# Kernel optimization log

Hardware: AMD Instinct MI355X
Metric: run time of the kernel (lower is better)

## Reference

```python
import jax, jax.numpy as jnp
import numpy as np

MARGIN = 0.3
LAMBDA_TRIPLET = 1.0
LAMBDA_ID = 1.0
EPS = 1e-6  # torch pairwise_distance eps added to the difference elementwise


def setup_inputs() -> dict:
    key = jax.random.key(0)
    k1, k2 = jax.random.split(key)
    B, N, D = 64, 512, 512
    reid_features = jax.random.normal(k1, (B, N, D), dtype=jnp.float32)
    # ids in [-1, 32): -1 marks invalid detections, as in the torch module
    track_ids = jax.random.randint(k2, (B, N), -1, 32, dtype=jnp.int32)
    return {"reid_features": reid_features, "track_ids": track_ids}


def _tracking_loss(feats, ids, margin):
    B, N, D = feats.shape
    valid = ids >= 0                                   # (B, N)
    same = ids[:, :, None] == ids[:, None, :]          # (B, N, N)
    not_self = ~jnp.eye(N, dtype=bool)                 # (N, N)
    valid_j = valid[:, None, :]                        # candidates must be valid
    pos_mask = same & not_self & valid_j               # (B, N, N)
    neg_mask = (~same) & valid_j                       # (B, N, N)
    has_pos = pos_mask.any(-1)                         # (B, N)
    has_neg = neg_mask.any(-1)
    enough = valid.sum(-1) >= 2                        # (B,)
    anchor_ok = valid & has_pos & has_neg & enough[:, None]
    # torch.nonzero(mask)[0] == first True index -> argmax on bool
    pos_idx = jnp.argmax(pos_mask, axis=-1)            # (B, N)
    neg_idx = jnp.argmax(neg_mask, axis=-1)
    p = jnp.take_along_axis(feats, pos_idx[..., None], axis=1)  # (B, N, D)
    n = jnp.take_along_axis(feats, neg_idx[..., None], axis=1)
    d_ap = jnp.sqrt(jnp.sum((feats - p + EPS) ** 2, axis=-1))   # (B, N)
    d_an = jnp.sqrt(jnp.sum((feats - n + EPS) ** 2, axis=-1))
    per_anchor = jnp.maximum(d_ap - d_an + margin, 0.0)
    num_triplets = anchor_ok.sum()
    total = jnp.sum(per_anchor * anchor_ok.astype(feats.dtype))
    loss = jnp.where(num_triplets > 0,
                     total / jnp.maximum(num_triplets, 1).astype(feats.dtype),
                     jnp.zeros((), feats.dtype))
    return loss * LAMBDA_TRIPLET


def reference(reid_features, track_ids):
    loss_triplet = _tracking_loss(reid_features, track_ids, MARGIN)
    loss_id = jnp.zeros((), reid_features.dtype)
    tracking_loss = loss_triplet + loss_id
    return tracking_loss, loss_triplet, loss_id
```

## Files before the change

### kernel.cpp

```cpp
#include <hip/hip_runtime.h>

#define MARGIN 0.3f
#define EPS 1e-6f

constexpr int B = 64, N = 512, D = 512;
constexpr int NIDS = 32;

constexpr int MB_THREADS = 256;
constexpr int MB_WAVES = MB_THREADS / 64;
constexpr int ANCH_PER_WAVE = 8;
constexpr int A_BLOCK = MB_WAVES * ANCH_PER_WAVE;
constexpr int MB_BLOCKS = (B * N) / A_BLOCK;


__global__ __launch_bounds__(512) void tl_tables(const int* __restrict__ ids,
                                                 int2* __restrict__ desc,
                                                 int2* __restrict__ hdr) {
    __shared__ int s_ids[N];
    __shared__ int s_first[NIDS], s_second[NIDS];
    __shared__ int s_j0, s_jdiff, s_vcnt;
    const int t = threadIdx.x;
    const int b = blockIdx.x;

    if (t < NIDS) { s_first[t] = N; s_second[t] = N; }
    if (t == 0) { s_j0 = N; s_jdiff = N; s_vcnt = 0; }
    __syncthreads();

    const int v = ids[b * N + t];
    s_ids[t] = v;
    const unsigned long long m = __ballot(v >= 0);
    if ((t & 63) == 0) atomicAdd(&s_vcnt, __popcll(m));
    if (v >= 0) {
        atomicMin(&s_first[v], t);
        atomicMin(&s_j0, t);
    }
    __syncthreads();
    const int id0 = (s_j0 < N) ? s_ids[s_j0] : -2;
    if (v >= 0) {
        if (s_first[v] != t) atomicMin(&s_second[v], t);
        if (v != id0) atomicMin(&s_jdiff, t);
    }
    __syncthreads();

    int2 d = make_int2(-1, -1);
    if (v >= 0 && s_vcnt >= 2) {
        const int posj = (s_first[v] != t) ? s_first[v] : s_second[v];
        const int negj = (v != id0) ? s_j0 : s_jdiff;
        if (posj < N && negj < N) d = make_int2(posj, negj);
    }
    desc[b * N + t] = d;
    if (t == 0) hdr[b] = make_int2(min(s_j0, N - 1), min(s_jdiff, N - 1));
}

__global__ __launch_bounds__(MB_THREADS) void tl_main(const float* __restrict__ feats,
                                                      const int2* __restrict__ desc,
                                                      const int2* __restrict__ hdr,
                                                      float* __restrict__ psum,
                                                      float* __restrict__ pcnt) {
    __shared__ int2 s_desc[A_BLOCK];
    __shared__ float s_wsum[MB_WAVES];
    __shared__ int s_wcnt[MB_WAVES];

    const int t = threadIdx.x;
    const int lane = t & 63;
    const int wave = t >> 6;

    const int logical = ((blockIdx.x & 7) << 7) | (blockIdx.x >> 3);
    const int b = logical >> 4;
    const int seg = (logical & 15) * A_BLOCK;
    const float* __restrict__ bf = feats + (size_t)b * N * D;

    if (t < A_BLOCK) s_desc[t] = desc[b * N + seg + t];

    const int2 h = hdr[b];
    const float4* n0p = (const float4*)(bf + (size_t)h.x * D) + lane * 2;
    const float4* n1p = (const float4*)(bf + (size_t)h.y * D) + lane * 2;
    const float4 n0a = n0p[0], n0b = n0p[1];
    const float4 n1a = n1p[0], n1b = n1p[1];

    __syncthreads();

    float wsum = 0.0f;
    int wcnt = 0;

    #pragma unroll
    for (int c = 0; c < ANCH_PER_WAVE / 4; ++c) {
        const int base = wave * ANCH_PER_WAVE + c * 4;

        int pj[4]; bool okk[4]; bool useN0[4];
        #pragma unroll
        for (int k = 0; k < 4; ++k) {
            const int2 d = s_desc[base + k];
            okk[k] = (d.x >= 0);
            pj[k] = okk[k] ? d.x : 0;
            useN0[k] = (d.y == h.x);
        }

        float4 A0[4], A1[4], P0[4], P1[4];
        #pragma unroll
        for (int k = 0; k < 4; ++k) {
            const int i = seg + base + k;
            const float4* fa = (const float4*)(bf + (size_t)i * D) + lane * 2;
            const float4* fp = (const float4*)(bf + (size_t)pj[k] * D) + lane * 2;
            A0[k] = fa[0]; A1[k] = fa[1];
            P0[k] = fp[0]; P1[k] = fp[1];
        }

        #pragma unroll
        for (int k = 0; k < 4; ++k) {
            const float4 m0 = useN0[k] ? n0a : n1a;
            const float4 m1 = useN0[k] ? n0b : n1b;
            float sap = 0.0f, san = 0.0f, dd;
            dd = A0[k].x - P0[k].x + EPS; sap += dd * dd;
            dd = A0[k].y - P0[k].y + EPS; sap += dd * dd;
            dd = A0[k].z - P0[k].z + EPS; sap += dd * dd;
            dd = A0[k].w - P0[k].w + EPS; sap += dd * dd;
            dd = A1[k].x - P1[k].x + EPS; sap += dd * dd;
            dd = A1[k].y - P1[k].y + EPS; sap += dd * dd;
            dd = A1[k].z - P1[k].z + EPS; sap += dd * dd;
            dd = A1[k].w - P1[k].w + EPS; sap += dd * dd;
            dd = A0[k].x - m0.x + EPS; san += dd * dd;
            dd = A0[k].y - m0.y + EPS; san += dd * dd;
            dd = A0[k].z - m0.z + EPS; san += dd * dd;
            dd = A0[k].w - m0.w + EPS; san += dd * dd;
            dd = A1[k].x - m1.x + EPS; san += dd * dd;
            dd = A1[k].y - m1.y + EPS; san += dd * dd;
            dd = A1[k].z - m1.z + EPS; san += dd * dd;
            dd = A1[k].w - m1.w + EPS; san += dd * dd;

            #pragma unroll
            for (int off = 32; off >= 1; off >>= 1) {
                sap += __shfl_xor(sap, off);
                san += __shfl_xor(san, off);
            }
            const float per = fmaxf(sqrtf(sap) - sqrtf(san) + MARGIN, 0.0f);
            wsum += okk[k] ? per : 0.0f;
            wcnt += okk[k] ? 1 : 0;
        }
    }

    if (lane == 0) { s_wsum[wave] = wsum; s_wcnt[wave] = wcnt; }
    __syncthreads();
    if (t == 0) {
        float s = 0.0f; int c = 0;
        #pragma unroll
        for (int w = 0; w < MB_WAVES; ++w) { s += s_wsum[w]; c += s_wcnt[w]; }
        psum[blockIdx.x] = s;
        pcnt[blockIdx.x] = (float)c;
    }
}

__global__ __launch_bounds__(256) void tl_finalize(const float* __restrict__ psum,
                                                   const float* __restrict__ pcnt,
                                                   float* __restrict__ out) {
    __shared__ float s_s[4], s_c[4];
    const int t = threadIdx.x;
    float s = 0.0f, c = 0.0f;
    for (int k = t; k < MB_BLOCKS; k += 256) { s += psum[k]; c += pcnt[k]; }
    #pragma unroll
    for (int off = 32; off >= 1; off >>= 1) {
        s += __shfl_xor(s, off);
        c += __shfl_xor(c, off);
    }
    if ((t & 63) == 0) { s_s[t >> 6] = s; s_c[t >> 6] = c; }
    __syncthreads();
    if (t == 0) {
        const float S = s_s[0] + s_s[1] + s_s[2] + s_s[3];
        const float C = s_c[0] + s_c[1] + s_c[2] + s_c[3];
        const float loss = (C > 0.0f) ? (S / C) : 0.0f;
        out[0] = loss;
        out[1] = loss;
        out[2] = 0.0f;
    }
}

extern "C" void kernel_launch(void* const* d_in, const int* in_sizes, int n_in,
                              void* d_out, int out_size, void* d_ws, size_t ws_size,
                              hipStream_t stream) {
    const float* feats = (const float*)d_in[0];
    const int* ids = (const int*)d_in[1];
    float* out = (float*)d_out;

    char* ws = (char*)d_ws;
    int2* desc = (int2*)ws;
    int2* hdr = (int2*)(ws + sizeof(int2) * B * N);
    float* psum = (float*)(ws + sizeof(int2) * (B * N + B));
    float* pcnt = psum + MB_BLOCKS;

    tl_tables<<<B, 512, 0, stream>>>(ids, desc, hdr);
    tl_main<<<MB_BLOCKS, MB_THREADS, 0, stream>>>(feats, desc, hdr, psum, pcnt);
    tl_finalize<<<1, 256, 0, stream>>>(psum, pcnt, out);
}
```

Measured before the change: 105.8 us.

## Fuse id-table construction into main triplet kernel with 512-thread blocks

Removes the separate tables kernel. Each main block now recomputes its batch's first/second-occurrence and negative tables in shared memory from the 512 ids, then derives positive and negative indices inline. Blocks grow to 512 threads so the whole id row can be loaded by one block, and the block-index swizzle is adjusted to match. This saves a kernel launch and the global desc/hdr round trip. In exchange, the table build is repeated by the eight blocks that share each batch, and the larger blocks may change occupancy.

```diff
diff --git a/kernel.cpp b/kernel.cpp
--- a/kernel.cpp
+++ b/kernel.cpp
@@ -6,21 +6,31 @@
 constexpr int B = 64, N = 512, D = 512;
 constexpr int NIDS = 32;
 
-constexpr int MB_THREADS = 256;
+constexpr int MB_THREADS = 512;
 constexpr int MB_WAVES = MB_THREADS / 64;
 constexpr int ANCH_PER_WAVE = 8;
 constexpr int A_BLOCK = MB_WAVES * ANCH_PER_WAVE;
 constexpr int MB_BLOCKS = (B * N) / A_BLOCK;
 
 
-__global__ __launch_bounds__(512) void tl_tables(const int* __restrict__ ids,
-                                                 int2* __restrict__ desc,
-                                                 int2* __restrict__ hdr) {
+__global__ __launch_bounds__(MB_THREADS) void tl_main(const float* __restrict__ feats,
+                                                      const int* __restrict__ ids,
+                                                      float* __restrict__ psum,
+                                                      float* __restrict__ pcnt) {
     __shared__ int s_ids[N];
     __shared__ int s_first[NIDS], s_second[NIDS];
     __shared__ int s_j0, s_jdiff, s_vcnt;
+    __shared__ float s_wsum[MB_WAVES];
+    __shared__ int s_wcnt[MB_WAVES];
+
     const int t = threadIdx.x;
-    const int b = blockIdx.x;
+    const int lane = t & 63;
+    const int wave = t >> 6;
+
+    const int logical = ((blockIdx.x & 7) << 6) | (blockIdx.x >> 3);
+    const int b = logical >> 3;
+    const int seg = (logical & 7) * A_BLOCK;
+    const float* __restrict__ bf = feats + (size_t)b * N * D;
 
     if (t < NIDS) { s_first[t] = N; s_second[t] = N; }
     if (t == 0) { s_j0 = N; s_jdiff = N; s_vcnt = 0; }
@@ -29,7 +39,7 @@
     const int v = ids[b * N + t];
     s_ids[t] = v;
     const unsigned long long m = __ballot(v >= 0);
-    if ((t & 63) == 0) atomicAdd(&s_vcnt, __popcll(m));
+    if (lane == 0) atomicAdd(&s_vcnt, __popcll(m));
     if (v >= 0) {
         atomicMin(&s_first[v], t);
         atomicMin(&s_j0, t);
@@ -42,64 +52,42 @@
     }
     __syncthreads();
 
-    int2 d = make_int2(-1, -1);
-    if (v >= 0 && s_vcnt >= 2) {
-        const int posj = (s_first[v] != t) ? s_first[v] : s_second[v];
-        const int negj = (v != id0) ? s_j0 : s_jdiff;
-        if (posj < N && negj < N) d = make_int2(posj, negj);
-    }
-    desc[b * N + t] = d;
-    if (t == 0) hdr[b] = make_int2(min(s_j0, N - 1), min(s_jdiff, N - 1));
-}
+    const int vcnt = s_vcnt;
+    const int j0 = min(s_j0, N - 1), jdiff = min(s_jdiff, N - 1);
 
-__global__ __launch_bounds__(MB_THREADS) void tl_main(const float* __restrict__ feats,
-                                                      const int2* __restrict__ desc,
-                                                      const int2* __restrict__ hdr,
-                                                      float* __restrict__ psum,
-                                                      float* __restrict__ pcnt) {
-    __shared__ int2 s_desc[A_BLOCK];
-    __shared__ float s_wsum[MB_WAVES];
-    __shared__ int s_wcnt[MB_WAVES];
-
-    const int t = threadIdx.x;
-    const int lane = t & 63;
-    const int wave = t >> 6;
-
-    const int logical = ((blockIdx.x & 7) << 7) | (blockIdx.x >> 3);
-    const int b = logical >> 4;
-    const int seg = (logical & 15) * A_BLOCK;
-    const float* __restrict__ bf = feats + (size_t)b * N * D;
-
-    if (t < A_BLOCK) s_desc[t] = desc[b * N + seg + t];
-
-    const int2 h = hdr[b];
-    const float4* n0p = (const float4*)(bf + (size_t)h.x * D) + lane * 2;
-    const float4* n1p = (const float4*)(bf + (size_t)h.y * D) + lane * 2;
+    const float4* n0p = (const float4*)(bf + (size_t)j0 * D) + lane * 2;
+    const float4* n1p = (const float4*)(bf + (size_t)jdiff * D) + lane * 2;
     const float4 n0a = n0p[0], n0b = n0p[1];
     const float4 n1a = n1p[0], n1b = n1p[1];
-
-    __syncthreads();
 
     float wsum = 0.0f;
     int wcnt = 0;
 
     #pragma unroll
     for (int c = 0; c < ANCH_PER_WAVE / 4; ++c) {
-        const int base = wave * ANCH_PER_WAVE + c * 4;
+        const int base = seg + wave * ANCH_PER_WAVE + c * 4;
 
         int pj[4]; bool okk[4]; bool useN0[4];
         #pragma unroll
         for (int k = 0; k < 4; ++k) {
-            const int2 d = s_desc[base + k];
-            okk[k] = (d.x >= 0);
-            pj[k] = okk[k] ? d.x : 0;
-            useN0[k] = (d.y == h.x);
+            const int i = base + k;
+            const int vi = s_ids[i];
+            bool ok = (vi >= 0) && (vcnt >= 2);
+            int posj = 0, negj = 0;
+            if (ok) {
+                posj = (s_first[vi] != i) ? s_first[vi] : s_second[vi];
+                negj = (vi != id0) ? s_j0 : s_jdiff;
+                ok = (posj < N) && (negj < N);
+            }
+            okk[k] = ok;
+            pj[k] = ok ? posj : 0;
+            useN0[k] = (negj == s_j0);
         }
 
         float4 A0[4], A1[4], P0[4], P1[4];
         #pragma unroll
         for (int k = 0; k < 4; ++k) {
-            const int i = seg + base + k;
+            const int i = base + k;
             const float4* fa = (const float4*)(bf + (size_t)i * D) + lane * 2;
             const float4* fp = (const float4*)(bf + (size_t)pj[k] * D) + lane * 2;
             A0[k] = fa[0]; A1[k] = fa[1];
@@ -181,13 +169,9 @@
     const int* ids = (const int*)d_in[1];
     float* out = (float*)d_out;
 
-    char* ws = (char*)d_ws;
-    int2* desc = (int2*)ws;
-    int2* hdr = (int2*)(ws + sizeof(int2) * B * N);
-    float* psum = (float*)(ws + sizeof(int2) * (B * N + B));
+    float* psum = (float*)d_ws;
     float* pcnt = psum + MB_BLOCKS;
 
-    tl_tables<<<B, 512, 0, stream>>>(ids, desc, hdr);
-    tl_main<<<MB_BLOCKS, MB_THREADS, 0, stream>>>(feats, desc, hdr, psum, pcnt);
+    tl_main<<<MB_BLOCKS, MB_THREADS, 0, stream>>>(feats, ids, psum, pcnt);
     tl_finalize<<<1, 256, 0, stream>>>(psum, pcnt, out);
 }
```

After: 103.3 us. -2.4%, faster.
